# Kernel optimization log

Hardware: AMD Instinct MI355X
Metric: run time of the kernel (lower is better)

The kernel has to match this reference:

```python
import jax, jax.numpy as jnp
import numpy as np

B, M, H = 512, 3, 768

def setup_inputs() -> dict:
    key = jax.random.key(0)
    ks = jax.random.split(key, 11)
    s = 1.0 / np.sqrt(H)
    return {
        "target": jax.random.normal(ks[0], (B, H), jnp.float32),
        "cont": jax.random.normal(ks[1], (B, M, H), jnp.float32),
        "Wq": jax.random.uniform(ks[2], (H, H), jnp.float32, -s, s),
        "bq": jax.random.uniform(ks[3], (H,), jnp.float32, -s, s),
        "Wk": jax.random.uniform(ks[4], (H, H), jnp.float32, -s, s),
        "bk": jax.random.uniform(ks[5], (H,), jnp.float32, -s, s),
        "Wv": jax.random.uniform(ks[6], (H, H), jnp.float32, -s, s),
        "bv": jax.random.uniform(ks[7], (H,), jnp.float32, -s, s),
        "p": jax.random.normal(ks[8], (M, H), jnp.float32),
        "h": jax.random.normal(ks[9], (M * H, M), jnp.float32),
        "g": jax.random.normal(ks[10], (M, H), jnp.float32),
    }

def reference(target, cont, Wq, bq, Wk, bk, Wv, bv, p, h, g):
    m = p.shape[0]
    hid = target.shape[-1]
    # torch nn.Linear: y = x @ W.T + b
    query = target @ Wq.T + bq                      # [B, H]
    key_ = cont @ Wk.T + bk                          # [B, m, H]
    value = cont @ Wv.T + bv                         # [B, m, H]
    # kernel_v = p @ query  -> [B, m]
    kernel_v = jnp.einsum('mh,bh->bm', p, query)
    # q = one @ query^T broadcasts query over the m rows, then * key
    x_q = query[:, None, :] * key_                   # [B, m, H]
    kernel_r = x_q.reshape(-1, m * hid) @ h          # [B, m]
    kernel = kernel_v + kernel_r                     # [B, m]
    # _xg = value^T @ g -> [B, H, H]
    _xg = jnp.einsum('bmh,mk->bhk', value, g)        # [B, H, H]
    x_nr = jnp.einsum('bmh,bhk->bmk', value, _xg)    # [B, m, H]
    context = x_nr + value                           # [B, m, H]
    output = jnp.einsum('bm,bmh->bh', kernel, context)  # [B, H]
    return output
```

## Files before the change

kernel.cpp:

```cpp
#include <hip/hip_runtime.h>
#include <hip/hip_bf16.h>

#define HID 768
#define NB  512
#define NM  3

typedef __bf16 bf16x8 __attribute__((ext_vector_type(8)));
typedef float  f32x4  __attribute__((ext_vector_type(4)));

#define WBF_OFF   1572864
#define QKV_OFF   1671168
#define QN        393216
#define KVN       1179648

__device__ __forceinline__ unsigned short f2bf(float f) {
    unsigned u = __builtin_bit_cast(unsigned, f);
    u += 0x7FFFu + ((u >> 16) & 1u);
    return (unsigned short)(u >> 16);
}

__device__ __forceinline__ void async_cp16(const void* g, void* l) {
    __builtin_amdgcn_global_load_lds(
        (const __attribute__((address_space(1))) void*)g,
        (__attribute__((address_space(3))) void*)l, 16, 0, 0);
}

__global__ __launch_bounds__(256) void cvt(
    const float4* __restrict__ t, const float4* __restrict__ c,
    const float4* __restrict__ wq, const float4* __restrict__ wk,
    const float4* __restrict__ wv, ushort4* __restrict__ abf,
    ushort4* __restrict__ wbf)
{
    int i = blockIdx.x * 256 + threadIdx.x;
    float4 v;
    ushort4* d;
    if (i < 393216) {
        v = (i < 98304) ? t[i] : c[i - 98304];
        d = abf + i;
    } else {
        int j = i - 393216;
        v = (j < 147456) ? wq[j] : (j < 294912 ? wk[j - 147456] : wv[j - 294912]);
        d = wbf + j;
    }
    ushort4 o = { f2bf(v.x), f2bf(v.y), f2bf(v.z), f2bf(v.w) };
    *d = o;
}

__global__ __launch_bounds__(256) void qkv_gemm(
    const unsigned short* __restrict__ bf, float* __restrict__ wsf,
    const float* __restrict__ bq, const float* __restrict__ bk,
    const float* __restrict__ bv)
{
    const unsigned short* Ab = bf;
    const unsigned short* Wb = bf + WBF_OFF;
    float* Qf = wsf + QKV_OFF;
    float* Kf = Qf + QN;
    float* Vf = Kf + KVN;

    int t = blockIdx.x;
    const unsigned short *A, *W;
    const float* bias;
    float* C;
    int mtiles;
    if (t < 96)       {          A = Ab;             W = Wb;              bias = bq; C = Qf; mtiles = 8;  }
    else if (t < 384) { t -= 96; A = Ab + 512 * HID; W = Wb + 768 * HID;  bias = bk; C = Kf; mtiles = 24; }
    else              { t -= 384; A = Ab + 512 * HID; W = Wb + 1536 * HID; bias = bv; C = Vf; mtiles = 24; }
    int tn = t / mtiles, tm = t % mtiles;
    int row0 = tm * 64, col0 = tn * 64;

    __shared__ unsigned short Al[64][32];
    __shared__ unsigned short Bl[64][32];

    int tid  = threadIdx.x;
    int l    = tid & 63;
    int w    = tid >> 6;
    int srow = tid >> 2;
    int scol = (tid & 3) * 8;

    const unsigned short* ga = A + (size_t)(row0 + srow) * HID + scol;
    const unsigned short* gb = W + (size_t)(col0 + srow) * HID + scol;
    char* la = (char*)&Al[0][0] + w * 1024;
    char* lb = (char*)&Bl[0][0] + w * 1024;

    int wm = (w & 1) * 32, wn = (w >> 1) * 32;
    int fm = l & 15, kof = (l >> 4) * 8;

    f32x4 acc00 = {0.f, 0.f, 0.f, 0.f};
    f32x4 acc01 = acc00, acc10 = acc00, acc11 = acc00;

    for (int k0 = 0; k0 < HID; k0 += 32) {
        __syncthreads();
        async_cp16(ga, la);
        async_cp16(gb, lb);
        ga += 32; gb += 32;
        __syncthreads();

        bf16x8 af0 = *(const bf16x8*)&Al[wm + fm][kof];
        bf16x8 af1 = *(const bf16x8*)&Al[wm + 16 + fm][kof];
        bf16x8 bf0 = *(const bf16x8*)&Bl[wn + fm][kof];
        bf16x8 bf1 = *(const bf16x8*)&Bl[wn + 16 + fm][kof];
        acc00 = __builtin_amdgcn_mfma_f32_16x16x32_bf16(af0, bf0, acc00, 0, 0, 0);
        acc01 = __builtin_amdgcn_mfma_f32_16x16x32_bf16(af0, bf1, acc01, 0, 0, 0);
        acc10 = __builtin_amdgcn_mfma_f32_16x16x32_bf16(af1, bf0, acc10, 0, 0, 0);
        acc11 = __builtin_amdgcn_mfma_f32_16x16x32_bf16(af1, bf1, acc11, 0, 0, 0);
    }

    int crow = row0 + wm + (l >> 4) * 4;
    int ccol = col0 + wn + fm;
    float bb0 = bias[ccol], bb1 = bias[ccol + 16];
    #pragma unroll
    for (int rg = 0; rg < 4; rg++) {
        C[(size_t)(crow + rg)      * HID + ccol]      = acc00[rg] + bb0;
        C[(size_t)(crow + rg)      * HID + ccol + 16] = acc01[rg] + bb1;
        C[(size_t)(crow + 16 + rg) * HID + ccol]      = acc10[rg] + bb0;
        C[(size_t)(crow + 16 + rg) * HID + ccol + 16] = acc11[rg] + bb1;
    }
}

__global__ __launch_bounds__(256) void finalize(
    const float* __restrict__ wsf, const float* __restrict__ p,
    const float* __restrict__ hmat, const float* __restrict__ g,
    float* __restrict__ out)
{
    int b    = blockIdx.x;
    int tid  = threadIdx.x;
    int lane = tid & 63;
    int wv   = tid >> 6;

    const float* q  = wsf + QKV_OFF + (size_t)b * HID;
    const float* kk = wsf + QKV_OFF + QN + (size_t)b * NM * HID;
    const float* vv = kk + KVN;

    float acc[12];
    #pragma unroll
    for (int i = 0; i < 12; i++) acc[i] = 0.f;

    for (int h0 = tid; h0 < HID; h0 += 256) {
        float qh = q[h0];
        float k0 = kk[h0], k1 = kk[HID + h0], k2 = kk[2 * HID + h0];
        float v0 = vv[h0], v1 = vv[HID + h0], v2 = vv[2 * HID + h0];
        acc[0] += p[h0] * qh;
        acc[1] += p[HID + h0] * qh;
        acc[2] += p[2 * HID + h0] * qh;
        float x0 = qh * k0, x1 = qh * k1, x2 = qh * k2;
        const float* h0p = hmat + (size_t)h0 * 3;
        const float* h1p = hmat + (size_t)(HID + h0) * 3;
        const float* h2p = hmat + (size_t)(2 * HID + h0) * 3;
        acc[3] += x0 * h0p[0] + x1 * h1p[0] + x2 * h2p[0];
        acc[4] += x0 * h0p[1] + x1 * h1p[1] + x2 * h2p[1];
        acc[5] += x0 * h0p[2] + x1 * h1p[2] + x2 * h2p[2];
        acc[6]  += v0 * v0; acc[7]  += v0 * v1; acc[8]  += v0 * v2;
        acc[9]  += v1 * v1; acc[10] += v1 * v2; acc[11] += v2 * v2;
    }

    #pragma unroll
    for (int i = 0; i < 12; i++)
        #pragma unroll
        for (int off = 32; off > 0; off >>= 1)
            acc[i] += __shfl_down(acc[i], off);

    __shared__ float sred[12][4];
    __shared__ float fin[12];
    if (lane == 0) {
        #pragma unroll
        for (int i = 0; i < 12; i++) sred[i][wv] = acc[i];
    }
    __syncthreads();
    if (tid < 12) fin[tid] = sred[tid][0] + sred[tid][1] + sred[tid][2] + sred[tid][3];
    __syncthreads();

    float kern0 = fin[0] + fin[3], kern1 = fin[1] + fin[4], kern2 = fin[2] + fin[5];
    float S00 = fin[6], S01 = fin[7], S02 = fin[8];
    float S11 = fin[9], S12 = fin[10], S22 = fin[11];

    for (int c = tid; c < HID; c += 256) {
        float g0 = g[c], g1 = g[HID + c], g2 = g[2 * HID + c];
        float v0 = vv[c], v1 = vv[HID + c], v2 = vv[2 * HID + c];
        float c0 = S00 * g0 + S01 * g1 + S02 * g2 + v0;
        float c1 = S01 * g0 + S11 * g1 + S12 * g2 + v1;
        float c2 = S02 * g0 + S12 * g1 + S22 * g2 + v2;
        out[(size_t)b * HID + c] = kern0 * c0 + kern1 * c1 + kern2 * c2;
    }
}

extern "C" void kernel_launch(void* const* d_in, const int* in_sizes, int n_in,
                              void* d_out, int out_size, void* d_ws, size_t ws_size,
                              hipStream_t stream) {
    (void)in_sizes; (void)n_in; (void)out_size; (void)ws_size;
    const float* target = (const float*)d_in[0];
    const float* cont   = (const float*)d_in[1];
    const float* Wq     = (const float*)d_in[2];
    const float* bq     = (const float*)d_in[3];
    const float* Wk     = (const float*)d_in[4];
    const float* bk     = (const float*)d_in[5];
    const float* Wv     = (const float*)d_in[6];
    const float* bv     = (const float*)d_in[7];
    const float* p      = (const float*)d_in[8];
    const float* hmat   = (const float*)d_in[9];
    const float* g      = (const float*)d_in[10];

    unsigned short* bfreg = (unsigned short*)d_ws;
    float* wsf = (float*)d_ws;
    float* out = (float*)d_out;

    cvt<<<3264, 256, 0, stream>>>((const float4*)target, (const float4*)cont,
                                  (const float4*)Wq, (const float4*)Wk, (const float4*)Wv,
                                  (ushort4*)bfreg, (ushort4*)(bfreg + WBF_OFF));
    qkv_gemm<<<672, 256, 0, stream>>>(bfreg, wsf, bq, bk, bv);
    finalize<<<512, 256, 0, stream>>>(wsf, p, hmat, g, out);
}
```

Before: 102.7 us.

## Double-buffer QKV GEMM with 128-wide K chunks and XOR-swizzled LDS

The QKV GEMM now stages 128-wide K chunks instead of 32-wide ones into two 32 KB LDS buffers, prefetching the next chunk while computing the current one. This cuts the number of barrier pairs per tile from 24 to about 6. An XOR swizzle on the LDS slot layout is meant to avoid bank conflicts on the 16-byte fragment reads. The cost is 64 KB of LDS per block, which limits how many blocks fit on a CU, and a more complex address computation. The finalize edits only rename variables.

```diff
diff --git a/kernel.cpp b/kernel.cpp
--- a/kernel.cpp
+++ b/kernel.cpp
@@ -47,12 +47,12 @@
 }
 
 __global__ __launch_bounds__(256) void qkv_gemm(
-    const unsigned short* __restrict__ bf, float* __restrict__ wsf,
+    const unsigned short* __restrict__ bfp, float* __restrict__ wsf,
     const float* __restrict__ bq, const float* __restrict__ bk,
     const float* __restrict__ bv)
 {
-    const unsigned short* Ab = bf;
-    const unsigned short* Wb = bf + WBF_OFF;
+    const unsigned short* Ab = bfp;
+    const unsigned short* Wb = bfp + WBF_OFF;
     float* Qf = wsf + QKV_OFF;
     float* Kf = Qf + QN;
     float* Vf = Kf + KVN;
@@ -62,50 +62,79 @@
     const float* bias;
     float* C;
     int mtiles;
-    if (t < 96)       {          A = Ab;             W = Wb;              bias = bq; C = Qf; mtiles = 8;  }
-    else if (t < 384) { t -= 96; A = Ab + 512 * HID; W = Wb + 768 * HID;  bias = bk; C = Kf; mtiles = 24; }
+    if (t < 96)       {          A = Ab;              W = Wb;              bias = bq; C = Qf; mtiles = 8;  }
+    else if (t < 384) { t -= 96;  A = Ab + 512 * HID; W = Wb + 768 * HID;  bias = bk; C = Kf; mtiles = 24; }
     else              { t -= 384; A = Ab + 512 * HID; W = Wb + 1536 * HID; bias = bv; C = Vf; mtiles = 24; }
     int tn = t / mtiles, tm = t % mtiles;
     int row0 = tm * 64, col0 = tn * 64;
 
-    __shared__ unsigned short Al[64][32];
-    __shared__ unsigned short Bl[64][32];
+    __shared__ __align__(16) unsigned short lds[32768];
+    char* ldsb = (char*)lds;
 
     int tid  = threadIdx.x;
-    int l    = tid & 63;
+    int lane = tid & 63;
     int w    = tid >> 6;
-    int srow = tid >> 2;
-    int scol = (tid & 3) * 8;
-
-    const unsigned short* ga = A + (size_t)(row0 + srow) * HID + scol;
-    const unsigned short* gb = W + (size_t)(col0 + srow) * HID + scol;
-    char* la = (char*)&Al[0][0] + w * 1024;
-    char* lb = (char*)&Bl[0][0] + w * 1024;
+    int q    = lane >> 4;
+    int fm   = lane & 15;
+
+    const unsigned short* gA[4];
+    const unsigned short* gB[4];
+    #pragma unroll
+    for (int j = 0; j < 4; j++) {
+        int r = j * 16 + w * 4 + q;
+        int g = fm ^ (r & 15);
+        gA[j] = A + (size_t)(row0 + r) * HID + g * 8;
+        gB[j] = W + (size_t)(col0 + r) * HID + g * 8;
+    }
 
     int wm = (w & 1) * 32, wn = (w >> 1) * 32;
-    int fm = l & 15, kof = (l >> 4) * 8;
 
     f32x4 acc00 = {0.f, 0.f, 0.f, 0.f};
     f32x4 acc01 = acc00, acc10 = acc00, acc11 = acc00;
 
-    for (int k0 = 0; k0 < HID; k0 += 32) {
-        __syncthreads();
-        async_cp16(ga, la);
-        async_cp16(gb, lb);
-        ga += 32; gb += 32;
-        __syncthreads();
-
-        bf16x8 af0 = *(const bf16x8*)&Al[wm + fm][kof];
-        bf16x8 af1 = *(const bf16x8*)&Al[wm + 16 + fm][kof];
-        bf16x8 bf0 = *(const bf16x8*)&Bl[wn + fm][kof];
-        bf16x8 bf1 = *(const bf16x8*)&Bl[wn + 16 + fm][kof];
-        acc00 = __builtin_amdgcn_mfma_f32_16x16x32_bf16(af0, bf0, acc00, 0, 0, 0);
-        acc01 = __builtin_amdgcn_mfma_f32_16x16x32_bf16(af0, bf1, acc01, 0, 0, 0);
-        acc10 = __builtin_amdgcn_mfma_f32_16x16x32_bf16(af1, bf0, acc10, 0, 0, 0);
-        acc11 = __builtin_amdgcn_mfma_f32_16x16x32_bf16(af1, bf1, acc11, 0, 0, 0);
-    }
-
-    int crow = row0 + wm + (l >> 4) * 4;
+    #define STAGE_LOAD(s, kc)                                            \
+        {                                                                \
+            char* bA_ = ldsb + (s) * 32768;                              \
+            char* bB_ = bA_ + 16384;                                     \
+            int ko_ = (kc) * 128;                                        \
+            _Pragma("unroll")                                            \
+            for (int j = 0; j < 4; j++) {                                \
+                async_cp16(gA[j] + ko_, bA_ + j * 4096 + w * 1024);      \
+                async_cp16(gB[j] + ko_, bB_ + j * 4096 + w * 1024);      \
+            }                                                            \
+        }
+
+    STAGE_LOAD(0, 0)
+    STAGE_LOAD(1, 1)
+    __syncthreads();
+
+    #pragma unroll
+    for (int c = 0; c < 6; c++) {
+        int s = c & 1;
+        char* bA = ldsb + s * 32768;
+        char* bB = bA + 16384;
+        #pragma unroll
+        for (int s4 = 0; s4 < 4; s4++) {
+            int slot = ((4 * s4 + q) ^ fm) * 16;
+            bf16x8 af0 = *(const bf16x8*)(bA + (wm + fm) * 256 + slot);
+            bf16x8 af1 = *(const bf16x8*)(bA + (wm + 16 + fm) * 256 + slot);
+            bf16x8 bf0 = *(const bf16x8*)(bB + (wn + fm) * 256 + slot);
+            bf16x8 bf1 = *(const bf16x8*)(bB + (wn + 16 + fm) * 256 + slot);
+            acc00 = __builtin_amdgcn_mfma_f32_16x16x32_bf16(af0, bf0, acc00, 0, 0, 0);
+            acc01 = __builtin_amdgcn_mfma_f32_16x16x32_bf16(af0, bf1, acc01, 0, 0, 0);
+            acc10 = __builtin_amdgcn_mfma_f32_16x16x32_bf16(af1, bf0, acc10, 0, 0, 0);
+            acc11 = __builtin_amdgcn_mfma_f32_16x16x32_bf16(af1, bf1, acc11, 0, 0, 0);
+        }
+        if (c < 4) {
+            __syncthreads();
+            STAGE_LOAD(s, c + 2)
+        } else if (c == 4) {
+            __syncthreads();
+        }
+    }
+    #undef STAGE_LOAD
+
+    int crow = row0 + wm + q * 4;
     int ccol = col0 + wn + fm;
     float bb0 = bias[ccol], bb1 = bias[ccol + 16];
     #pragma unroll
@@ -127,16 +156,16 @@
     int lane = tid & 63;
     int wv   = tid >> 6;
 
-    const float* q  = wsf + QKV_OFF + (size_t)b * HID;
-    const float* kk = wsf + QKV_OFF + QN + (size_t)b * NM * HID;
-    const float* vv = kk + KVN;
+    const float* qrow = wsf + QKV_OFF + (size_t)b * HID;
+    const float* kk   = wsf + QKV_OFF + QN + (size_t)b * NM * HID;
+    const float* vv   = kk + KVN;
 
     float acc[12];
     #pragma unroll
     for (int i = 0; i < 12; i++) acc[i] = 0.f;
 
     for (int h0 = tid; h0 < HID; h0 += 256) {
-        float qh = q[h0];
+        float qh = qrow[h0];
         float k0 = kk[h0], k1 = kk[HID + h0], k2 = kk[2 * HID + h0];
         float v0 = vv[h0], v1 = vv[HID + h0], v2 = vv[2 * HID + h0];
         acc[0] += p[h0] * qh;
@@ -173,13 +202,13 @@
     float S00 = fin[6], S01 = fin[7], S02 = fin[8];
     float S11 = fin[9], S12 = fin[10], S22 = fin[11];
 
-    for (int c = tid; c < HID; c += 256) {
-        float g0 = g[c], g1 = g[HID + c], g2 = g[2 * HID + c];
-        float v0 = vv[c], v1 = vv[HID + c], v2 = vv[2 * HID + c];
+    for (int cc = tid; cc < HID; cc += 256) {
+        float g0 = g[cc], g1 = g[HID + cc], g2 = g[2 * HID + cc];
+        float v0 = vv[cc], v1 = vv[HID + cc], v2 = vv[2 * HID + cc];
         float c0 = S00 * g0 + S01 * g1 + S02 * g2 + v0;
         float c1 = S01 * g0 + S11 * g1 + S12 * g2 + v1;
         float c2 = S02 * g0 + S12 * g1 + S22 * g2 + v2;
-        out[(size_t)b * HID + c] = kern0 * c0 + kern1 * c1 + kern2 * c2;
+        out[(size_t)b * HID + cc] = kern0 * c0 + kern1 * c1 + kern2 * c2;
     }
 }
 
```

Result: no change. 102.8 us, median of 2 (+0.0%).
